# Kernel optimization log

Measured on AMD Instinct MI355X. Metric: run time of the kernel, lower is better.

## Reference

```python
import jax, jax.numpy as jnp
import numpy as np

TAU = 0.1
EPS_NORM = 1e-12
EPS_DENOM = 1e-8


def _l2norm(x):
    # F.normalize(x, dim=1): x / max(||x||, eps)
    n = jnp.linalg.norm(x, axis=1, keepdims=True)
    return x / jnp.maximum(n, EPS_NORM)


def setup_inputs() -> dict:
    key = jax.random.key(0)
    ks = jax.random.split(key, 8)
    D, N_POS, N_HARD, N_MIX = 512, 8192, 65536, 64
    return {
        "anchor": jax.random.normal(ks[0], (1, D), dtype=jnp.float32),
        "positives": jax.random.normal(ks[1], (N_POS, D), dtype=jnp.float32),
        "hard_negatives": jax.random.normal(ks[2], (N_HARD, D), dtype=jnp.float32),
        "mix_idx": jax.random.randint(ks[3], (N_MIX,), 0, N_HARD, dtype=jnp.int32),
        "idx_a": jax.random.randint(ks[4], (N_MIX,), 0, N_HARD, dtype=jnp.int32),
        "idx_b": jax.random.randint(ks[5], (N_MIX,), 0, N_HARD, dtype=jnp.int32),
        "alpha_raw": jax.random.uniform(ks[6], (N_MIX, 1), dtype=jnp.float32),
        "beta_raw": jax.random.uniform(ks[7], (N_MIX, 1), dtype=jnp.float32),
    }


def reference(anchor, positives, hard_negatives, mix_idx, idx_a, idx_b, alpha_raw, beta_raw):
    a = _l2norm(anchor)            # [1, D]
    p = _l2norm(positives)         # [N_pos, D]
    h = _l2norm(hard_negatives)    # [N_hard, D]

    # MoCHi synthesis: anchor-mixed hardest negatives
    alpha = alpha_raw * 0.4 + 0.1                      # [N_mix, 1] in [0.1, 0.5)
    hardest = _l2norm((1.0 - alpha) * h[mix_idx] + alpha * a)
    # negative-negative mixes
    beta = beta_raw * 0.4 + 0.3                        # [N_mix, 1] in [0.3, 0.7)
    harder = _l2norm(beta * h[idx_a] + (1.0 - beta) * h[idx_b])

    all_negs = jnp.concatenate([h, hardest, harder], axis=0)  # [N_hard + 128, D]

    av = a[0]                                  # [D]
    pos_logits = (p @ av) / TAU                # [N_pos]
    neg_logits = (all_negs @ av) / TAU         # [N_neg]

    neg_sum_exp = jnp.sum(jnp.exp(neg_logits))
    pos_val = jnp.exp(pos_logits)
    # original: mean_i of -log(exp(l_i) / (exp(l_i) + neg_sum_exp + 1e-8))
    loss = jnp.mean(-jnp.log(pos_val / (pos_val + neg_sum_exp + EPS_DENOM)))
    return loss
```

## Files before the change

kernel.cpp:

```cpp
#include <hip/hip_runtime.h>
#include <math.h>

#define TAU_F       0.1f
#define EPS_NORM_F  1e-12f
#define EPS_DENOM_F 1e-8f

__device__ __forceinline__ float dot4(float4 a, float4 b) {
    return a.x * b.x + a.y * b.y + a.z * b.z + a.w * b.w;
}

__global__ void __launch_bounds__(256) main_kernel(
        const float* __restrict__ anchor,
        const float* __restrict__ pos,
        const float* __restrict__ hn,
        const int* __restrict__ mix_idx,
        const int* __restrict__ idx_a,
        const int* __restrict__ idx_b,
        const float* __restrict__ alpha_raw,
        const float* __restrict__ beta_raw,
        double* __restrict__ S_acc,
        float* __restrict__ cos_p,
        int n_hard, int n_pos, int n_mix) {
    const int lane = threadIdx.x & 63;
    const int wib  = threadIdx.x >> 6;
    const int wpb  = blockDim.x >> 6;
    const int wid  = blockIdx.x * wpb + wib;
    const int nw   = gridDim.x * wpb;

    const float4* a4 = (const float4*)anchor;
    const float4 a0 = a4[lane];
    const float4 a1 = a4[lane + 64];
    float na2 = dot4(a0, a0) + dot4(a1, a1);
    #pragma unroll
    for (int o = 32; o > 0; o >>= 1) na2 += __shfl_xor(na2, o, 64);
    const float na = fmaxf(sqrtf(na2), EPS_NORM_F);

    const int total = n_hard + n_pos;
    const int per   = (total + nw - 1) / nw;
    const int base  = wid * per;

    float local_exp = 0.0f;

    for (int it = 0; it < per; it += 3) {
        const int r0 = base + it;
        const int r1 = r0 + 1;
        const int r2 = r0 + 2;
        const int c0 = r0 < total ? r0 : 0;
        const int c1 = r1 < total ? r1 : 0;
        const int c2 = r2 < total ? r2 : 0;
        const float4* p0 = (c0 < n_hard) ? (const float4*)hn  + (size_t)c0 * 128
                                         : (const float4*)pos + (size_t)(c0 - n_hard) * 128;
        const float4* p1 = (c1 < n_hard) ? (const float4*)hn  + (size_t)c1 * 128
                                         : (const float4*)pos + (size_t)(c1 - n_hard) * 128;
        const float4* p2 = (c2 < n_hard) ? (const float4*)hn  + (size_t)c2 * 128
                                         : (const float4*)pos + (size_t)(c2 - n_hard) * 128;
        const float4 v00 = p0[lane], v01 = p0[lane + 64];
        const float4 v10 = p1[lane], v11 = p1[lane + 64];
        const float4 v20 = p2[lane], v21 = p2[lane + 64];

        float s0 = dot4(v00, a0) + dot4(v01, a1);
        float q0 = dot4(v00, v00) + dot4(v01, v01);
        float s1 = dot4(v10, a0) + dot4(v11, a1);
        float q1 = dot4(v10, v10) + dot4(v11, v11);
        float s2 = dot4(v20, a0) + dot4(v21, a1);
        float q2 = dot4(v20, v20) + dot4(v21, v21);

        #pragma unroll
        for (int o = 32; o > 0; o >>= 1) {
            s0 += __shfl_xor(s0, o, 64);  q0 += __shfl_xor(q0, o, 64);
            s1 += __shfl_xor(s1, o, 64);  q1 += __shfl_xor(q1, o, 64);
            s2 += __shfl_xor(s2, o, 64);  q2 += __shfl_xor(q2, o, 64);
        }

        const float cos0 = s0 / (fmaxf(sqrtf(q0), EPS_NORM_F) * na);
        const float cos1 = s1 / (fmaxf(sqrtf(q1), EPS_NORM_F) * na);
        const float cos2 = s2 / (fmaxf(sqrtf(q2), EPS_NORM_F) * na);

        if (r0 < total) {
            if (r0 < n_hard) local_exp += expf(cos0 / TAU_F);
            else if (lane == 0) cos_p[r0 - n_hard] = cos0;
        }
        if (r1 < total) {
            if (r1 < n_hard) local_exp += expf(cos1 / TAU_F);
            else if (lane == 0) cos_p[r1 - n_hard] = cos1;
        }
        if (r2 < total) {
            if (r2 < n_hard) local_exp += expf(cos2 / TAU_F);
            else if (lane == 0) cos_p[r2 - n_hard] = cos2;
        }
    }

    if (wid < n_mix) {
        const int j = wid;
        const float4* R = (const float4*)hn + (size_t)mix_idx[j] * 128;
        const float4 v0 = R[lane], v1 = R[lane + 64];
        float s  = dot4(v0, a0) + dot4(v1, a1);
        float n2 = dot4(v0, v0) + dot4(v1, v1);
        #pragma unroll
        for (int o = 32; o > 0; o >>= 1) {
            s  += __shfl_xor(s,  o, 64);
            n2 += __shfl_xor(n2, o, 64);
        }
        const float nrm = fmaxf(sqrtf(n2), EPS_NORM_F);
        const float c   = s / (nrm * na);
        const float al  = alpha_raw[j] * 0.4f + 0.1f;
        const float num  = (1.0f - al) * c + al;
        const float den2 = (1.0f - al) * (1.0f - al) + al * al
                         + 2.0f * al * (1.0f - al) * c;
        const float cosm = num / fmaxf(sqrtf(den2), EPS_NORM_F);
        local_exp += expf(cosm / TAU_F);
    } else if (wid < 2 * n_mix) {
        const int k  = wid - n_mix;
        const float4* A = (const float4*)hn + (size_t)idx_a[k] * 128;
        const float4* B = (const float4*)hn + (size_t)idx_b[k] * 128;
        const float4 x0 = A[lane], x1 = A[lane + 64];
        const float4 y0 = B[lane], y1 = B[lane + 64];
        float sa  = dot4(x0, a0) + dot4(x1, a1);
        float sb  = dot4(y0, a0) + dot4(y1, a1);
        float d   = dot4(x0, y0) + dot4(x1, y1);
        float nA2 = dot4(x0, x0) + dot4(x1, x1);
        float nB2 = dot4(y0, y0) + dot4(y1, y1);
        #pragma unroll
        for (int o = 32; o > 0; o >>= 1) {
            sa  += __shfl_xor(sa,  o, 64);
            sb  += __shfl_xor(sb,  o, 64);
            d   += __shfl_xor(d,   o, 64);
            nA2 += __shfl_xor(nA2, o, 64);
            nB2 += __shfl_xor(nB2, o, 64);
        }
        const float nA  = fmaxf(sqrtf(nA2), EPS_NORM_F);
        const float nB  = fmaxf(sqrtf(nB2), EPS_NORM_F);
        const float ca  = sa / (nA * na);
        const float cb  = sb / (nB * na);
        const float dab = d  / (nA * nB);
        const float be  = beta_raw[k] * 0.4f + 0.3f;
        const float num  = be * ca + (1.0f - be) * cb;
        const float den2 = be * be + (1.0f - be) * (1.0f - be)
                         + 2.0f * be * (1.0f - be) * dab;
        const float cosm = num / fmaxf(sqrtf(den2), EPS_NORM_F);
        local_exp += expf(cosm / TAU_F);
    }

    __shared__ float sred[16];
    if (lane == 0) sred[wib] = local_exp;
    __syncthreads();
    if (threadIdx.x == 0) {
        float t = 0.0f;
        for (int i = 0; i < wpb; ++i) t += sred[i];
        atomicAdd(S_acc, (double)t);
    }
}

__global__ void __launch_bounds__(256) finish_kernel(
        const float* __restrict__ cos_p,
        const double* __restrict__ S_acc,
        float* __restrict__ out,
        int n_pos) {
    __shared__ double sred[256];
    const float S = (float)S_acc[0];
    double acc = 0.0;
    for (int i = threadIdx.x; i < n_pos; i += blockDim.x) {
        const float pv = expf(cos_p[i] / TAU_F);
        acc += (double)(-logf(pv / (pv + S + EPS_DENOM_F)));
    }
    sred[threadIdx.x] = acc;
    __syncthreads();
    for (int s = blockDim.x >> 1; s > 0; s >>= 1) {
        if (threadIdx.x < (unsigned)s) sred[threadIdx.x] += sred[threadIdx.x + s];
        __syncthreads();
    }
    if (threadIdx.x == 0) out[0] = (float)(sred[0] / (double)n_pos);
}

extern "C" void kernel_launch(void* const* d_in, const int* in_sizes, int n_in,
                              void* d_out, int out_size, void* d_ws, size_t ws_size,
                              hipStream_t stream) {
    const float* anchor    = (const float*)d_in[0];
    const float* positives = (const float*)d_in[1];
    const float* hardnegs  = (const float*)d_in[2];
    const int*   mix_idx   = (const int*)d_in[3];
    const int*   idx_a     = (const int*)d_in[4];
    const int*   idx_b     = (const int*)d_in[5];
    const float* alpha_raw = (const float*)d_in[6];
    const float* beta_raw  = (const float*)d_in[7];

    const int D      = in_sizes[0];
    const int n_pos  = in_sizes[1] / D;
    const int n_hard = in_sizes[2] / D;
    const int n_mix  = in_sizes[3];

    char*   ws    = (char*)d_ws;
    double* S_acc = (double*)ws;
    float*  cos_p = (float*)(ws + 1024);

    hipMemsetAsync(S_acc, 0, sizeof(double), stream);

    main_kernel<<<2048, 256, 0, stream>>>(anchor, positives, hardnegs,
                                          mix_idx, idx_a, idx_b,
                                          alpha_raw, beta_raw,
                                          S_acc, cos_p, n_hard, n_pos, n_mix);

    finish_kernel<<<1, 256, 0, stream>>>(cos_p, S_acc, (float*)d_out, n_pos);
}
```

Before: 234.4 us.

## Software-pipeline row loads and replace atomic accumulation with per-block partial sums

The main loop gets a specialized path for exactly nine rows per wave. The next three rows are loaded before the current three are reduced, so memory latency overlaps the shuffle reductions. The double atomicAdd and memset are replaced by per-block partial sums that a wider 1024-thread finish kernel reduces before computing the positive-log terms. This removes atomic contention and one memset launch, at the cost of higher register pressure in the pipelined path and a larger final reduction.

```diff
diff --git a/kernel.cpp b/kernel.cpp
--- a/kernel.cpp
+++ b/kernel.cpp
@@ -7,6 +7,40 @@
 
 __device__ __forceinline__ float dot4(float4 a, float4 b) {
     return a.x * b.x + a.y * b.y + a.z * b.z + a.w * b.w;
+}
+
+__device__ __forceinline__ const float4* rowptr(int r, int n_hard,
+        const float4* __restrict__ hn4, const float4* __restrict__ pos4) {
+    return (r < n_hard) ? hn4 + (size_t)r * 128
+                        : pos4 + (size_t)(r - n_hard) * 128;
+}
+
+__device__ __forceinline__ void reduce3(
+        int r0, int r1, int r2, int n_hard,
+        float4 v00, float4 v01, float4 v10, float4 v11, float4 v20, float4 v21,
+        float4 a0, float4 a1, float na, int lane,
+        float& local_exp, float* __restrict__ cos_p) {
+    float s0 = dot4(v00, a0) + dot4(v01, a1);
+    float q0 = dot4(v00, v00) + dot4(v01, v01);
+    float s1 = dot4(v10, a0) + dot4(v11, a1);
+    float q1 = dot4(v10, v10) + dot4(v11, v11);
+    float s2 = dot4(v20, a0) + dot4(v21, a1);
+    float q2 = dot4(v20, v20) + dot4(v21, v21);
+    #pragma unroll
+    for (int o = 32; o > 0; o >>= 1) {
+        s0 += __shfl_xor(s0, o, 64);  q0 += __shfl_xor(q0, o, 64);
+        s1 += __shfl_xor(s1, o, 64);  q1 += __shfl_xor(q1, o, 64);
+        s2 += __shfl_xor(s2, o, 64);  q2 += __shfl_xor(q2, o, 64);
+    }
+    const float c0 = s0 / (fmaxf(sqrtf(q0), EPS_NORM_F) * na);
+    const float c1 = s1 / (fmaxf(sqrtf(q1), EPS_NORM_F) * na);
+    const float c2 = s2 / (fmaxf(sqrtf(q2), EPS_NORM_F) * na);
+    if (r0 < n_hard) local_exp += expf(c0 / TAU_F);
+    else if (lane == 0) cos_p[r0 - n_hard] = c0;
+    if (r1 < n_hard) local_exp += expf(c1 / TAU_F);
+    else if (lane == 0) cos_p[r1 - n_hard] = c1;
+    if (r2 < n_hard) local_exp += expf(c2 / TAU_F);
+    else if (lane == 0) cos_p[r2 - n_hard] = c2;
 }
 
 __global__ void __launch_bounds__(256) main_kernel(
@@ -18,7 +52,7 @@
         const int* __restrict__ idx_b,
         const float* __restrict__ alpha_raw,
         const float* __restrict__ beta_raw,
-        double* __restrict__ S_acc,
+        double* __restrict__ block_sums,
         float* __restrict__ cos_p,
         int n_hard, int n_pos, int n_mix) {
     const int lane = threadIdx.x & 63;
@@ -27,6 +61,9 @@
     const int wid  = blockIdx.x * wpb + wib;
     const int nw   = gridDim.x * wpb;
 
+    const float4* hn4  = (const float4*)hn;
+    const float4* pos4 = (const float4*)pos;
+
     const float4* a4 = (const float4*)anchor;
     const float4 a0 = a4[lane];
     const float4 a1 = a4[lane + 64];
@@ -41,58 +78,59 @@
 
     float local_exp = 0.0f;
 
-    for (int it = 0; it < per; it += 3) {
-        const int r0 = base + it;
-        const int r1 = r0 + 1;
-        const int r2 = r0 + 2;
-        const int c0 = r0 < total ? r0 : 0;
-        const int c1 = r1 < total ? r1 : 0;
-        const int c2 = r2 < total ? r2 : 0;
-        const float4* p0 = (c0 < n_hard) ? (const float4*)hn  + (size_t)c0 * 128
-                                         : (const float4*)pos + (size_t)(c0 - n_hard) * 128;
-        const float4* p1 = (c1 < n_hard) ? (const float4*)hn  + (size_t)c1 * 128
-                                         : (const float4*)pos + (size_t)(c1 - n_hard) * 128;
-        const float4* p2 = (c2 < n_hard) ? (const float4*)hn  + (size_t)c2 * 128
-                                         : (const float4*)pos + (size_t)(c2 - n_hard) * 128;
-        const float4 v00 = p0[lane], v01 = p0[lane + 64];
-        const float4 v10 = p1[lane], v11 = p1[lane + 64];
-        const float4 v20 = p2[lane], v21 = p2[lane + 64];
-
-        float s0 = dot4(v00, a0) + dot4(v01, a1);
-        float q0 = dot4(v00, v00) + dot4(v01, v01);
-        float s1 = dot4(v10, a0) + dot4(v11, a1);
-        float q1 = dot4(v10, v10) + dot4(v11, v11);
-        float s2 = dot4(v20, a0) + dot4(v21, a1);
-        float q2 = dot4(v20, v20) + dot4(v21, v21);
-
-        #pragma unroll
-        for (int o = 32; o > 0; o >>= 1) {
-            s0 += __shfl_xor(s0, o, 64);  q0 += __shfl_xor(q0, o, 64);
-            s1 += __shfl_xor(s1, o, 64);  q1 += __shfl_xor(q1, o, 64);
-            s2 += __shfl_xor(s2, o, 64);  q2 += __shfl_xor(q2, o, 64);
-        }
-
-        const float cos0 = s0 / (fmaxf(sqrtf(q0), EPS_NORM_F) * na);
-        const float cos1 = s1 / (fmaxf(sqrtf(q1), EPS_NORM_F) * na);
-        const float cos2 = s2 / (fmaxf(sqrtf(q2), EPS_NORM_F) * na);
-
-        if (r0 < total) {
-            if (r0 < n_hard) local_exp += expf(cos0 / TAU_F);
-            else if (lane == 0) cos_p[r0 - n_hard] = cos0;
-        }
-        if (r1 < total) {
-            if (r1 < n_hard) local_exp += expf(cos1 / TAU_F);
-            else if (lane == 0) cos_p[r1 - n_hard] = cos1;
-        }
-        if (r2 < total) {
-            if (r2 < n_hard) local_exp += expf(cos2 / TAU_F);
-            else if (lane == 0) cos_p[r2 - n_hard] = cos2;
+    if (per == 9 && base + 9 <= total) {
+        const float4* P0 = rowptr(base + 0, n_hard, hn4, pos4);
+        const float4* P1 = rowptr(base + 1, n_hard, hn4, pos4);
+        const float4* P2 = rowptr(base + 2, n_hard, hn4, pos4);
+        const float4* P3 = rowptr(base + 3, n_hard, hn4, pos4);
+        const float4* P4 = rowptr(base + 4, n_hard, hn4, pos4);
+        const float4* P5 = rowptr(base + 5, n_hard, hn4, pos4);
+        float4 A00 = P0[lane], A01 = P0[lane + 64];
+        float4 A10 = P1[lane], A11 = P1[lane + 64];
+        float4 A20 = P2[lane], A21 = P2[lane + 64];
+        float4 B00 = P3[lane], B01 = P3[lane + 64];
+        float4 B10 = P4[lane], B11 = P4[lane + 64];
+        float4 B20 = P5[lane], B21 = P5[lane + 64];
+
+        reduce3(base + 0, base + 1, base + 2, n_hard,
+                A00, A01, A10, A11, A20, A21, a0, a1, na, lane,
+                local_exp, cos_p);
+
+        const float4* P6 = rowptr(base + 6, n_hard, hn4, pos4);
+        const float4* P7 = rowptr(base + 7, n_hard, hn4, pos4);
+        const float4* P8 = rowptr(base + 8, n_hard, hn4, pos4);
+        A00 = P6[lane]; A01 = P6[lane + 64];
+        A10 = P7[lane]; A11 = P7[lane + 64];
+        A20 = P8[lane]; A21 = P8[lane + 64];
+
+        reduce3(base + 3, base + 4, base + 5, n_hard,
+                B00, B01, B10, B11, B20, B21, a0, a1, na, lane,
+                local_exp, cos_p);
+
+        reduce3(base + 6, base + 7, base + 8, n_hard,
+                A00, A01, A10, A11, A20, A21, a0, a1, na, lane,
+                local_exp, cos_p);
+    } else {
+        for (int it = 0; it < per; ++it) {
+            const int r = base + it;
+            if (r >= total) break;
+            const float4* P = rowptr(r, n_hard, hn4, pos4);
+            const float4 v0 = P[lane], v1 = P[lane + 64];
+            float s  = dot4(v0, a0) + dot4(v1, a1);
+            float q  = dot4(v0, v0) + dot4(v1, v1);
+            #pragma unroll
+            for (int o = 32; o > 0; o >>= 1) {
+                s += __shfl_xor(s, o, 64);  q += __shfl_xor(q, o, 64);
+            }
+            const float c = s / (fmaxf(sqrtf(q), EPS_NORM_F) * na);
+            if (r < n_hard) local_exp += expf(c / TAU_F);
+            else if (lane == 0) cos_p[r - n_hard] = c;
         }
     }
 
     if (wid < n_mix) {
         const int j = wid;
-        const float4* R = (const float4*)hn + (size_t)mix_idx[j] * 128;
+        const float4* R = hn4 + (size_t)mix_idx[j] * 128;
         const float4 v0 = R[lane], v1 = R[lane + 64];
         float s  = dot4(v0, a0) + dot4(v1, a1);
         float n2 = dot4(v0, v0) + dot4(v1, v1);
@@ -111,8 +149,8 @@
         local_exp += expf(cosm / TAU_F);
     } else if (wid < 2 * n_mix) {
         const int k  = wid - n_mix;
-        const float4* A = (const float4*)hn + (size_t)idx_a[k] * 128;
-        const float4* B = (const float4*)hn + (size_t)idx_b[k] * 128;
+        const float4* A = hn4 + (size_t)idx_a[k] * 128;
+        const float4* B = hn4 + (size_t)idx_b[k] * 128;
         const float4 x0 = A[lane], x1 = A[lane + 64];
         const float4 y0 = B[lane], y1 = B[lane + 64];
         float sa  = dot4(x0, a0) + dot4(x1, a1);
@@ -147,25 +185,34 @@
     if (threadIdx.x == 0) {
         float t = 0.0f;
         for (int i = 0; i < wpb; ++i) t += sred[i];
-        atomicAdd(S_acc, (double)t);
-    }
-}
-
-__global__ void __launch_bounds__(256) finish_kernel(
-        const float* __restrict__ cos_p,
-        const double* __restrict__ S_acc,
-        float* __restrict__ out,
-        int n_pos) {
-    __shared__ double sred[256];
-    const float S = (float)S_acc[0];
+        block_sums[blockIdx.x] = (double)t;
+    }
+}
+
+__global__ void __launch_bounds__(1024) finish_kernel(
+        const double* __restrict__ block_sums, int nblocks,
+        const float* __restrict__ cos_p, int n_pos,
+        float* __restrict__ out) {
+    __shared__ double sred[1024];
     double acc = 0.0;
-    for (int i = threadIdx.x; i < n_pos; i += blockDim.x) {
+    for (int i = threadIdx.x; i < nblocks; i += 1024) acc += block_sums[i];
+    sred[threadIdx.x] = acc;
+    __syncthreads();
+    for (int s = 512; s > 0; s >>= 1) {
+        if (threadIdx.x < (unsigned)s) sred[threadIdx.x] += sred[threadIdx.x + s];
+        __syncthreads();
+    }
+    const float S = (float)sred[0];
+    __syncthreads();
+
+    double lacc = 0.0;
+    for (int i = threadIdx.x; i < n_pos; i += 1024) {
         const float pv = expf(cos_p[i] / TAU_F);
-        acc += (double)(-logf(pv / (pv + S + EPS_DENOM_F)));
-    }
-    sred[threadIdx.x] = acc;
-    __syncthreads();
-    for (int s = blockDim.x >> 1; s > 0; s >>= 1) {
+        lacc += (double)(-logf(pv / (pv + S + EPS_DENOM_F)));
+    }
+    sred[threadIdx.x] = lacc;
+    __syncthreads();
+    for (int s = 512; s > 0; s >>= 1) {
         if (threadIdx.x < (unsigned)s) sred[threadIdx.x] += sred[threadIdx.x + s];
         __syncthreads();
     }
@@ -189,16 +236,18 @@
     const int n_hard = in_sizes[2] / D;
     const int n_mix  = in_sizes[3];
 
-    char*   ws    = (char*)d_ws;
-    double* S_acc = (double*)ws;
-    float*  cos_p = (float*)(ws + 1024);
-
-    hipMemsetAsync(S_acc, 0, sizeof(double), stream);
-
-    main_kernel<<<2048, 256, 0, stream>>>(anchor, positives, hardnegs,
+    const int GRID = 2048;
+
+    char*   ws         = (char*)d_ws;
+    double* block_sums = (double*)ws;
+    float*  cos_p      = (float*)(ws + (size_t)GRID * sizeof(double));
+
+    main_kernel<<<GRID, 256, 0, stream>>>(anchor, positives, hardnegs,
                                           mix_idx, idx_a, idx_b,
                                           alpha_raw, beta_raw,
-                                          S_acc, cos_p, n_hard, n_pos, n_mix);
-
-    finish_kernel<<<1, 256, 0, stream>>>(cos_p, S_acc, (float*)d_out, n_pos);
-}
+                                          block_sums, cos_p,
+                                          n_hard, n_pos, n_mix);
+
+    finish_kernel<<<1, 1024, 0, stream>>>(block_sums, GRID, cos_p,
+                                          n_pos, (float*)d_out);
+}
```

Result: faster. 221.4 us (-5.6%).
